# Kernel tuning notes

Measured on AMD Instinct MI355X. Metric: run time of the kernel, lower is better.

Reference implementation:

```python
import jax, jax.numpy as jnp
from jax import lax
import numpy as np

EPS = 0.15      # constraint_value_upper_bound (per-row box |y/c - 1| <= EPS)
DELTA = 0.05    # groups_constraint_upper_bound (per-group mean |y/c - 1| <= DELTA)
N_GROUPS = 8
N_ITERS = 300   # Dykstra iterations; converges to the exact QP projection

N, D, H1, H2, K = 65536, 512, 1024, 512, 1


def setup_inputs() -> dict:
    key = jax.random.key(0)
    ks = jax.random.split(key, 8)
    x = jax.random.normal(ks[0], (N, D), jnp.float32)
    W1 = jax.random.normal(ks[1], (D, H1), jnp.float32) / np.float32(np.sqrt(D))
    b1 = jnp.zeros((H1,), jnp.float32)
    W2 = jax.random.normal(ks[2], (H1, H2), jnp.float32) / np.float32(np.sqrt(H1))
    b2 = jnp.zeros((H2,), jnp.float32)
    Wf = jax.random.normal(ks[3], (H2, K), jnp.float32) / np.float32(np.sqrt(H2))
    bf = jnp.zeros((K,), jnp.float32)
    c = jax.random.uniform(ks[4], (N,), jnp.float32, 0.5, 2.0)
    # quantiles_price_tensor: q_i = (1/N) * #{k : c_k <= c_i}  (rank via searchsorted)
    q = jnp.searchsorted(jnp.sort(c), c, side='right').astype(jnp.float32) / N
    # group j covers q in [j/G, (j+1)/G]; assign boundary ties to the lower group
    g = jnp.clip(jnp.ceil(q * N_GROUPS).astype(jnp.int32) - 1, 0, N_GROUPS - 1)
    group_mask = jax.nn.one_hot(g, N_GROUPS, dtype=jnp.float32).T  # [G, N]
    return dict(x=x, W1=W1, b1=b1, W2=W2, b2=b2, Wf=Wf, bf=bf,
                constraint_constant=c, group_mask=group_mask)


def _project(y_u, c, group_mask):
    """Exact QP: min ||y - y_u||^2 s.t. |y_i/c_i - 1| <= EPS and
    |mean_{i in G_j}(y_i/c_i - 1)| <= DELTA, solved by Dykstra's alternating
    projections in z = y/c - 1 space under the weighted norm sum c_i^2 z_i^2."""
    w = c * c                                   # [N] weights of the norm
    z0 = y_u / c[:, None] - 1.0                 # [N, K]
    n = group_mask.sum(axis=1)                  # [G] group sizes
    a = group_mask / n[:, None]                 # [G, N] averaging rows
    denom = (a * a / w[None, :]).sum(axis=1)    # [G]  a^T W^{-1} a
    u = (a / w[None, :]) / denom[:, None]       # [G, N] weighted slab directions

    def proj_box(z):
        return jnp.clip(z, -EPS, EPS)

    def proj_grp(z):
        v = a @ z                               # [G, K] group means
        return z - u.T @ (v - jnp.clip(v, -DELTA, DELTA))

    def body(carry, _):
        z, p, q = carry
        zb = proj_box(z + p); p = z + p - zb
        zg = proj_grp(zb + q); q = zb + q - zg
        return (zg, p, q), None

    init = (z0, jnp.zeros_like(z0), jnp.zeros_like(z0))
    (z, _, _), _ = lax.scan(body, init, None, length=N_ITERS)
    return (z + 1.0) * c[:, None]


def reference(x, W1, b1, W2, b2, Wf, bf, constraint_constant, group_mask):
    h = jax.nn.relu(x @ W1 + b1)   # Dropout is identity in eval mode
    h = jax.nn.relu(h @ W2 + b2)
    y_u = h @ Wf + bf              # [N, 1] unconstrained predictions
    return _project(y_u, constraint_constant, group_mask)
```

## Files before the change

kernel.cpp:

```cpp
#include <hip/hip_runtime.h>
#include <hip/hip_bf16.h>

#define NROWS 65536
#define DIM   512
#define H1DIM 1024
#define H2DIM 512
#define EPSC  0.15f
#define DELTA 0.05f
#define NGRP  8
#define CAPG  16384

typedef __bf16 bf16x8 __attribute__((ext_vector_type(8)));
typedef float  f32x4  __attribute__((ext_vector_type(4)));

__device__ __forceinline__ void gload16(const void* g, void* lds) {
  __builtin_amdgcn_global_load_lds((__attribute__((address_space(1))) const unsigned int*)g,
                                   (__attribute__((address_space(3))) unsigned int*)lds,
                                   16, 0, 0);
}

__global__ void k_zero(float* y_u, int n, int* cnt) {
  int i = blockIdx.x * blockDim.x + threadIdx.x;
  if (i < n) y_u[i] = 0.f;
  if (i < NGRP) cnt[i] = 0;
}

__global__ void k_tcvt(const float* __restrict__ src, __bf16* __restrict__ dst, int R, int C) {
  __shared__ float tile[32][33];
  const int bi = blockIdx.x * 32;
  const int bj = blockIdx.y * 32;
  const int tx = threadIdx.x, ty = threadIdx.y;
  #pragma unroll
  for (int r = ty; r < 32; r += 8)
    tile[r][tx] = src[(size_t)(bi + r) * C + bj + tx];
  __syncthreads();
  #pragma unroll
  for (int r = ty; r < 32; r += 8)
    dst[(size_t)(bj + r) * R + bi + tx] = (__bf16)tile[tx][r];
}

__global__ __launch_bounds__(256) void k_cvt_x(const float4* __restrict__ x4,
                                               bf16x8* __restrict__ xb8, int n8) {
  int i = blockIdx.x * blockDim.x + threadIdx.x;
  const int stride = gridDim.x * blockDim.x;
  for (; i < n8; i += stride) {
    const float4 a = x4[2 * i];
    const float4 b = x4[2 * i + 1];
    bf16x8 v;
    v[0] = (__bf16)a.x; v[1] = (__bf16)a.y; v[2] = (__bf16)a.z; v[3] = (__bf16)a.w;
    v[4] = (__bf16)b.x; v[5] = (__bf16)b.y; v[6] = (__bf16)b.z; v[7] = (__bf16)b.w;
    xb8[i] = v;
  }
}

__global__ __launch_bounds__(512, 2) void k_gemm1(const __bf16* __restrict__ xb,
                                                  const __bf16* __restrict__ w1t,
                                                  const float* __restrict__ b1,
                                                  __bf16* __restrict__ h1) {
  __shared__ __align__(16) __bf16 As[2][256 * 64];
  __shared__ __align__(16) __bf16 Bs[2][256 * 64];
  const int tid = threadIdx.x;
  const int w = tid >> 6, l = tid & 63;
  const int mt   = (int)gridDim.x >> 2;
  const int mper = mt >> 3;
  const int xcd  = blockIdx.x & 7;
  const int idx  = blockIdx.x >> 3;
  const int brow = (xcd * mper + (idx >> 2)) * 256;
  const int bcol = (idx & 3) * 256;
  const int lr = l & 15, lk = l >> 4;
  const int wm = w >> 2, wn = w & 3;
  const int mbase = wm * 128, nbase = wn * 64;
  const int srow = w * 32 + (l >> 3);
  const int scol = (l & 7) * 8;
  const int NT = DIM / 64;
  f32x4 acc[8][4] = {};

  #define STAGE1(KT, BUF) do { \
    _Pragma("unroll") for (int t_ = 0; t_ < 4; ++t_) { \
      gload16(xb  + (size_t)(brow + srow + t_ * 8) * DIM + (KT) + scol, \
              As[BUF] + (w * 32 + t_ * 8) * 64); \
      gload16(w1t + (size_t)(bcol + srow + t_ * 8) * DIM + (KT) + scol, \
              Bs[BUF] + (w * 32 + t_ * 8) * 64); } } while (0)
  #define COMPUTE1(BUF) do { \
    _Pragma("unroll") for (int kk = 0; kk < 64; kk += 32) { \
      bf16x8 af[8], bq[4]; \
      _Pragma("unroll") for (int m = 0; m < 8; ++m) \
        af[m] = *(const bf16x8*)(As[BUF] + (mbase + m * 16 + lr) * 64 + kk + lk * 8); \
      _Pragma("unroll") for (int nn = 0; nn < 4; ++nn) \
        bq[nn] = *(const bf16x8*)(Bs[BUF] + (nbase + nn * 16 + lr) * 64 + kk + lk * 8); \
      __builtin_amdgcn_s_setprio(1); \
      _Pragma("unroll") for (int m = 0; m < 8; ++m) \
        _Pragma("unroll") for (int nn = 0; nn < 4; ++nn) \
          acc[m][nn] = __builtin_amdgcn_mfma_f32_16x16x32_bf16(af[m], bq[nn], acc[m][nn], 0, 0, 0); \
      __builtin_amdgcn_s_setprio(0); \
    } } while (0)

  STAGE1(0, 0);
  __syncthreads();
  int cur = 0;
  for (int t = 0; t < NT - 1; ++t) {
    STAGE1((t + 1) * 64, cur ^ 1);
    COMPUTE1(cur);
    __syncthreads();
    cur ^= 1;
  }
  COMPUTE1(cur);

  #undef STAGE1
  #undef COMPUTE1

  #pragma unroll
  for (int nn = 0; nn < 4; ++nn) {
    const int col = bcol + nbase + nn * 16 + lr;
    const float bias = b1[col];
    #pragma unroll
    for (int m = 0; m < 8; ++m) {
      const int row = brow + mbase + m * 16 + lk * 4;
      #pragma unroll
      for (int j = 0; j < 4; ++j) {
        float v = acc[m][nn][j] + bias;
        v = fmaxf(v, 0.f);
        h1[(size_t)(row + j) * H1DIM + col] = (__bf16)v;
      }
    }
  }
}

__global__ __launch_bounds__(512, 2) void k_gemm2(const __bf16* __restrict__ h1,
                                                  const __bf16* __restrict__ w2t,
                                                  const float* __restrict__ b2,
                                                  const float* __restrict__ wf,
                                                  float* __restrict__ y_u, int row0) {
  __shared__ __align__(16) __bf16 As[2][256 * 64];
  __shared__ __align__(16) __bf16 Bs[2][256 * 64];
  __shared__ float yred[256];
  const int tid = threadIdx.x;
  const int w = tid >> 6, l = tid & 63;
  const int mt   = (int)gridDim.x >> 1;
  const int mper = mt >> 3;
  const int xcd  = blockIdx.x & 7;
  const int idx  = blockIdx.x >> 3;
  const int brow = (xcd * mper + (idx >> 1)) * 256;
  const int n0   = (idx & 1) * 256;
  const int lr = l & 15, lk = l >> 4;
  const int wm = w >> 2, wn = w & 3;
  const int mbase = wm * 128, nbase = wn * 64;
  const int srow = w * 32 + (l >> 3);
  const int scol = (l & 7) * 8;
  const int NT = H1DIM / 64;
  f32x4 acc[8][4] = {};

  #define STAGE2(KT, BUF) do { \
    _Pragma("unroll") for (int t_ = 0; t_ < 4; ++t_) { \
      gload16(h1  + (size_t)(brow + srow + t_ * 8) * H1DIM + (KT) + scol, \
              As[BUF] + (w * 32 + t_ * 8) * 64); \
      gload16(w2t + (size_t)(n0   + srow + t_ * 8) * H1DIM + (KT) + scol, \
              Bs[BUF] + (w * 32 + t_ * 8) * 64); } } while (0)
  #define COMPUTE2(BUF) do { \
    _Pragma("unroll") for (int kk = 0; kk < 64; kk += 32) { \
      bf16x8 af[8], bq[4]; \
      _Pragma("unroll") for (int m = 0; m < 8; ++m) \
        af[m] = *(const bf16x8*)(As[BUF] + (mbase + m * 16 + lr) * 64 + kk + lk * 8); \
      _Pragma("unroll") for (int nn = 0; nn < 4; ++nn) \
        bq[nn] = *(const bf16x8*)(Bs[BUF] + (nbase + nn * 16 + lr) * 64 + kk + lk * 8); \
      __builtin_amdgcn_s_setprio(1); \
      _Pragma("unroll") for (int m = 0; m < 8; ++m) \
        _Pragma("unroll") for (int nn = 0; nn < 4; ++nn) \
          acc[m][nn] = __builtin_amdgcn_mfma_f32_16x16x32_bf16(af[m], bq[nn], acc[m][nn], 0, 0, 0); \
      __builtin_amdgcn_s_setprio(0); \
    } } while (0)

  STAGE2(0, 0);
  __syncthreads();
  int cur = 0;
  for (int t = 0; t < NT - 1; ++t) {
    STAGE2((t + 1) * 64, cur ^ 1);
    COMPUTE2(cur);
    __syncthreads();
    cur ^= 1;
  }
  COMPUTE2(cur);

  #undef STAGE2
  #undef COMPUTE2

  float yacc[8][4] = {};
  #pragma unroll
  for (int nn = 0; nn < 4; ++nn) {
    const int col = n0 + nbase + nn * 16 + lr;
    const float bias = b2[col];
    const float wfv = wf[col];
    #pragma unroll
    for (int m = 0; m < 8; ++m)
      #pragma unroll
      for (int j = 0; j < 4; ++j)
        yacc[m][j] += fmaxf(acc[m][nn][j] + bias, 0.f) * wfv;
  }
  #pragma unroll
  for (int m = 0; m < 8; ++m)
    #pragma unroll
    for (int j = 0; j < 4; ++j) {
      float v = yacc[m][j];
      v += __shfl_xor(v, 1, 64);
      v += __shfl_xor(v, 2, 64);
      v += __shfl_xor(v, 4, 64);
      v += __shfl_xor(v, 8, 64);
      yacc[m][j] = v;
    }
  if (tid < 256) yred[tid] = 0.f;
  __syncthreads();
  if (lr == 0) {
    #pragma unroll
    for (int m = 0; m < 8; ++m)
      #pragma unroll
      for (int j = 0; j < 4; ++j)
        atomicAdd(&yred[mbase + m * 16 + lk * 4 + j], yacc[m][j]);
  }
  __syncthreads();
  if (tid < 256) atomicAdd(&y_u[row0 + brow + tid], yred[tid]);
}

__global__ __launch_bounds__(256) void k_scatter(const float* __restrict__ y_u,
                                                 const float* __restrict__ c,
                                                 const float* __restrict__ mask,
                                                 const float* __restrict__ bfp,
                                                 float* __restrict__ z0c, float* __restrict__ wc,
                                                 unsigned char* __restrict__ gidx,
                                                 int* __restrict__ cnt, int n) {
  __shared__ int lcnt[NGRP];
  __shared__ int lbase[NGRP];
  const float bf0 = bfp[0];
  const int tid = threadIdx.x;
  if (tid < NGRP) lcnt[tid] = 0;
  __syncthreads();
  const int i = blockIdx.x * blockDim.x + tid;
  int g = 0, slot_l = 0;
  float z0 = 0.f, wv = 0.f;
  if (i < n) {
    const float cv = c[i];
    z0 = (y_u[i] + bf0) / cv - 1.f;
    wv = cv * cv;
    #pragma unroll
    for (int j = 1; j < NGRP; ++j)
      if (mask[(size_t)j * NROWS + i] > 0.5f) g = j;
    slot_l = atomicAdd(&lcnt[g], 1);
    gidx[i] = (unsigned char)g;
  }
  __syncthreads();
  if (tid < NGRP) lbase[tid] = atomicAdd(&cnt[tid], lcnt[tid]);
  __syncthreads();
  if (i < n) {
    const int slot = lbase[g] + slot_l;
    if (slot < CAPG) {
      z0c[(size_t)g * CAPG + slot] = z0;
      wc [(size_t)g * CAPG + slot] = wv;
    }
  }
}

__device__ __forceinline__ float wave_red(float v, int mode) {
  #pragma unroll
  for (int o = 32; o > 0; o >>= 1) {
    float u = __shfl_xor(v, o, 64);
    v = (mode == 0) ? (v + u) : ((mode == 1) ? fmaxf(v, u) : fminf(v, u));
  }
  return v;
}
__device__ __forceinline__ float block_red(float v, int mode, float* red, int tid) {
  v = wave_red(v, mode);
  if ((tid & 63) == 0) red[tid >> 6] = v;
  __syncthreads();
  if (tid < 64) {
    float x = (tid < 16) ? red[tid] : (mode == 0 ? 0.f : (mode == 1 ? -1e30f : 1e30f));
    x = wave_red(x, mode);
    if (tid == 0) red[0] = x;
  }
  __syncthreads();
  float r = red[0];
  __syncthreads();
  return r;
}

__global__ __launch_bounds__(1024) void k_mu(const float* __restrict__ z0c,
                                             const float* __restrict__ wc,
                                             const int* __restrict__ cnt,
                                             float* __restrict__ muarr) {
  __shared__ float red[16];
  const int g = blockIdx.x;
  const int tid = threadIdx.x;
  int n = cnt[g];
  if (n > CAPG) n = CAPG;
  if (n <= 0) { if (tid == 0) muarr[g] = 0.f; return; }
  float z0v[16], iwv[16];
  float hmax = -1e30f, hmin = 1e30f;
  #pragma unroll
  for (int t = 0; t < 16; ++t) {
    const int idx = t * 1024 + tid;
    if (idx < n) {
      const float z0 = z0c[(size_t)g * CAPG + idx];
      const float wv = wc[(size_t)g * CAPG + idx];
      z0v[t] = z0; iwv[t] = 1.f / wv;
      hmax = fmaxf(hmax, (z0 + EPSC) * wv);
      hmin = fminf(hmin, (z0 - EPSC) * wv);
    } else { z0v[t] = 0.f; iwv[t] = 0.f; }
  }
  const float inv_n = 1.f / (float)n;
  #define EVALM(MU, OUT) do { float s_ = 0.f; \
    _Pragma("unroll") for (int t = 0; t < 16; ++t) \
      s_ += fminf(fmaxf(z0v[t] - (MU) * iwv[t], -EPSC), EPSC); \
    OUT = block_red(s_, 0, red, tid) * inv_n; } while (0)
  float m0; EVALM(0.f, m0);
  float mu = 0.f;
  if (fabsf(m0) > DELTA) {
    float target, lo, hi;
    if (m0 > 0.f) { target = DELTA;  lo = 0.f; hi = block_red(hmax, 1, red, tid); }
    else          { target = -DELTA; hi = 0.f; lo = block_red(hmin, 2, red, tid); }
    for (int it = 0; it < 32; ++it) {
      const float mid = 0.5f * (lo + hi);
      float mm; EVALM(mid, mm);
      if (mm >= target) lo = mid; else hi = mid;
    }
    mu = 0.5f * (lo + hi);
  }
  if (tid == 0) muarr[g] = mu;
  #undef EVALM
}

__global__ void k_y(const float* __restrict__ y_u, const float* __restrict__ c,
                    const float* __restrict__ bfp, const unsigned char* __restrict__ gidx,
                    const float* __restrict__ muarr, float* __restrict__ out, int n) {
  const float bf0 = bfp[0];
  int i = blockIdx.x * blockDim.x + threadIdx.x;
  const int stride = gridDim.x * blockDim.x;
  for (; i < n; i += stride) {
    const float cv = c[i];
    const float z0 = (y_u[i] + bf0) / cv - 1.f;
    const float wv = cv * cv;
    const float mu = muarr[gidx[i]];
    const float z = fminf(fmaxf(z0 - mu / wv, -EPSC), EPSC);
    out[i] = (z + 1.f) * cv;
  }
}

extern "C" void kernel_launch(void* const* d_in, const int* in_sizes, int n_in,
                              void* d_out, int out_size, void* d_ws, size_t ws_size,
                              hipStream_t stream) {
  const float* x    = (const float*)d_in[0];
  const float* W1   = (const float*)d_in[1];
  const float* b1   = (const float*)d_in[2];
  const float* W2   = (const float*)d_in[3];
  const float* b2   = (const float*)d_in[4];
  const float* Wf   = (const float*)d_in[5];
  const float* bfp  = (const float*)d_in[6];
  const float* c    = (const float*)d_in[7];
  const float* mask = (const float*)d_in[8];
  float* out = (float*)d_out;

  char* ws = (char*)d_ws;
  size_t off = 0;
  auto alloc = [&](size_t bytes) -> void* {
    void* p = ws + off;
    off += (bytes + 255) & ~(size_t)255;
    return p;
  };
  __bf16* w1t = (__bf16*)alloc((size_t)H1DIM * DIM * 2);
  __bf16* w2t = (__bf16*)alloc((size_t)H2DIM * H1DIM * 2);
  float* y_u  = (float*)alloc((size_t)NROWS * 4);
  float* z0c  = (float*)alloc((size_t)NGRP * CAPG * 4);
  float* wc   = (float*)alloc((size_t)NGRP * CAPG * 4);
  unsigned char* gidx = (unsigned char*)alloc(NROWS);
  int*   cnt  = (int*)alloc(NGRP * 4);
  float* muarr = (float*)alloc(NGRP * 4);
  const size_t fixed = off;

  size_t avail = (ws_size > fixed) ? (ws_size - fixed) : 0;
  long long rc = (long long)(avail / ((size_t)(DIM + H1DIM * 2)));
  rc &= ~2047LL;
  if (rc > 32768) rc = 32768;
  if (rc < 2048) rc = 2048;
  const int rows_chunk = (int)rc;
  __bf16* xb = (__bf16*)(ws + fixed);
  __bf16* h1 = (__bf16*)(ws + fixed + (size_t)rows_chunk * DIM * 2);

  k_zero<<<dim3((NROWS + 255) / 256), dim3(256), 0, stream>>>(y_u, NROWS, cnt);
  k_tcvt<<<dim3(DIM / 32, H1DIM / 32), dim3(32, 8), 0, stream>>>(W1, w1t, DIM, H1DIM);
  k_tcvt<<<dim3(H1DIM / 32, H2DIM / 32), dim3(32, 8), 0, stream>>>(W2, w2t, H1DIM, H2DIM);

  for (int r0 = 0; r0 < NROWS; r0 += rows_chunk) {
    const int Mc = (NROWS - r0 < rows_chunk) ? (NROWS - r0) : rows_chunk;
    const int mtiles = Mc / 256;
    const int n8 = Mc * (DIM / 8);
    int cblocks = (n8 + 255) / 256; if (cblocks > 2048) cblocks = 2048;
    k_cvt_x<<<dim3(cblocks), dim3(256), 0, stream>>>(
        (const float4*)(x + (size_t)r0 * DIM), (bf16x8*)xb, n8);
    k_gemm1<<<dim3(mtiles * 4), dim3(512), 0, stream>>>(xb, w1t, b1, h1);
    k_gemm2<<<dim3(mtiles * 2), dim3(512), 0, stream>>>(h1, w2t, b2, Wf, y_u, r0);
  }

  k_scatter<<<dim3((NROWS + 255) / 256), dim3(256), 0, stream>>>(y_u, c, mask, bfp, z0c, wc, gidx, cnt, NROWS);
  k_mu<<<dim3(NGRP), dim3(1024), 0, stream>>>(z0c, wc, cnt, muarr);
  k_y<<<dim3(256), dim3(256), 0, stream>>>(y_u, c, bfp, gidx, muarr, out, NROWS);
}
```

Measured before the change: 273.5 us.

## Swizzle GEMM LDS tiles and overlap next-tile loads with compute via vmcnt waits

Both GEMM kernels now XOR-swizzle the 16-byte chunks of each LDS row, on the global-to-LDS store side and on the MFMA fragment read side, to cut LDS bank conflicts. The blanket __syncthreads is replaced by explicit s_waitcnt vmcnt(8) plus raw barriers, so the current tile is consumed while the next tile's 8 async loads stay in flight. This relies on getting the vmcnt accounting and LDS visibility right by hand. If the counts are wrong, the kernels could read stale data.

```diff
diff --git a/kernel.cpp b/kernel.cpp
--- a/kernel.cpp
+++ b/kernel.cpp
@@ -52,6 +52,7 @@
     xb8[i] = v;
   }
 }
+
 
 __global__ __launch_bounds__(512, 2) void k_gemm1(const __bf16* __restrict__ xb,
                                                   const __bf16* __restrict__ w1t,
@@ -71,7 +72,8 @@
   const int wm = w >> 2, wn = w & 3;
   const int mbase = wm * 128, nbase = wn * 64;
   const int srow = w * 32 + (l >> 3);
-  const int scol = (l & 7) * 8;
+  const int scol = (((l & 7) ^ ((l >> 3) & 7)) * 8);
+  const int swz  = (lr & 7) << 4;
   const int NT = DIM / 64;
   f32x4 acc[8][4] = {};
 
@@ -85,9 +87,11 @@
     _Pragma("unroll") for (int kk = 0; kk < 64; kk += 32) { \
       bf16x8 af[8], bq[4]; \
       _Pragma("unroll") for (int m = 0; m < 8; ++m) \
-        af[m] = *(const bf16x8*)(As[BUF] + (mbase + m * 16 + lr) * 64 + kk + lk * 8); \
+        af[m] = *(const bf16x8*)((const char*)(As[BUF]) + \
+                 ((((mbase + m * 16 + lr) * 128) + kk * 2 + lk * 16) ^ swz)); \
       _Pragma("unroll") for (int nn = 0; nn < 4; ++nn) \
-        bq[nn] = *(const bf16x8*)(Bs[BUF] + (nbase + nn * 16 + lr) * 64 + kk + lk * 8); \
+        bq[nn] = *(const bf16x8*)((const char*)(Bs[BUF]) + \
+                 ((((nbase + nn * 16 + lr) * 128) + kk * 2 + lk * 16) ^ swz)); \
       __builtin_amdgcn_s_setprio(1); \
       _Pragma("unroll") for (int m = 0; m < 8; ++m) \
         _Pragma("unroll") for (int nn = 0; nn < 4; ++nn) \
@@ -96,14 +100,17 @@
     } } while (0)
 
   STAGE1(0, 0);
-  __syncthreads();
   int cur = 0;
   for (int t = 0; t < NT - 1; ++t) {
     STAGE1((t + 1) * 64, cur ^ 1);
+    asm volatile("s_waitcnt vmcnt(8)" ::: "memory");
+    __builtin_amdgcn_s_barrier();
     COMPUTE1(cur);
-    __syncthreads();
+    __builtin_amdgcn_s_barrier();
     cur ^= 1;
   }
+  asm volatile("s_waitcnt vmcnt(0)" ::: "memory");
+  __builtin_amdgcn_s_barrier();
   COMPUTE1(cur);
 
   #undef STAGE1
@@ -146,7 +153,8 @@
   const int wm = w >> 2, wn = w & 3;
   const int mbase = wm * 128, nbase = wn * 64;
   const int srow = w * 32 + (l >> 3);
-  const int scol = (l & 7) * 8;
+  const int scol = (((l & 7) ^ ((l >> 3) & 7)) * 8);
+  const int swz  = (lr & 7) << 4;
   const int NT = H1DIM / 64;
   f32x4 acc[8][4] = {};
 
@@ -160,9 +168,11 @@
     _Pragma("unroll") for (int kk = 0; kk < 64; kk += 32) { \
       bf16x8 af[8], bq[4]; \
       _Pragma("unroll") for (int m = 0; m < 8; ++m) \
-        af[m] = *(const bf16x8*)(As[BUF] + (mbase + m * 16 + lr) * 64 + kk + lk * 8); \
+        af[m] = *(const bf16x8*)((const char*)(As[BUF]) + \
+                 ((((mbase + m * 16 + lr) * 128) + kk * 2 + lk * 16) ^ swz)); \
       _Pragma("unroll") for (int nn = 0; nn < 4; ++nn) \
-        bq[nn] = *(const bf16x8*)(Bs[BUF] + (nbase + nn * 16 + lr) * 64 + kk + lk * 8); \
+        bq[nn] = *(const bf16x8*)((const char*)(Bs[BUF]) + \
+                 ((((nbase + nn * 16 + lr) * 128) + kk * 2 + lk * 16) ^ swz)); \
       __builtin_amdgcn_s_setprio(1); \
       _Pragma("unroll") for (int m = 0; m < 8; ++m) \
         _Pragma("unroll") for (int nn = 0; nn < 4; ++nn) \
@@ -171,14 +181,17 @@
     } } while (0)
 
   STAGE2(0, 0);
-  __syncthreads();
   int cur = 0;
   for (int t = 0; t < NT - 1; ++t) {
     STAGE2((t + 1) * 64, cur ^ 1);
+    asm volatile("s_waitcnt vmcnt(8)" ::: "memory");
+    __builtin_amdgcn_s_barrier();
     COMPUTE2(cur);
-    __syncthreads();
+    __builtin_amdgcn_s_barrier();
     cur ^= 1;
   }
+  asm volatile("s_waitcnt vmcnt(0)" ::: "memory");
+  __builtin_amdgcn_s_barrier();
   COMPUTE2(cur);
 
   #undef STAGE2
```

After: 242.0 us. 11.5% less time.
